# Kernel optimization log

Measured on AMD Instinct MI355X. Metric: run time of the kernel, lower is better.

The kernel has to match this reference:

```python
import jax, jax.numpy as jnp
import numpy as np

D_MODEL = 1024
NUM_HEADS = 16
D_K = D_MODEL // NUM_HEADS
THETA = 10000.0
MAX_SEQ_LEN = 2048
BATCH = 2
SEQ = 2048


def setup_inputs() -> dict:
    key = jax.random.key(0)
    ks = jax.random.split(key, 5)
    std = np.sqrt(2.0 / (D_MODEL + D_MODEL)).astype(np.float32)
    x = jax.random.normal(ks[0], (BATCH, SEQ, D_MODEL), dtype=jnp.float32)
    Wq = jax.random.normal(ks[1], (D_MODEL, D_MODEL), dtype=jnp.float32) * std
    Wk = jax.random.normal(ks[2], (D_MODEL, D_MODEL), dtype=jnp.float32) * std
    Wv = jax.random.normal(ks[3], (D_MODEL, D_MODEL), dtype=jnp.float32) * std
    Wo = jax.random.normal(ks[4], (D_MODEL, D_MODEL), dtype=jnp.float32) * std
    token_positions = jnp.arange(SEQ, dtype=jnp.int32)
    return {"x": x, "token_positions": token_positions,
            "Wq": Wq, "Wk": Wk, "Wv": Wv, "Wo": Wo}


def _rope_tables(positions):
    # freqs: [d_k/2]; angles: [seq, d_k/2]
    freqs = 1.0 / (THETA ** (jnp.arange(0, D_K, 2, dtype=jnp.float32) / D_K))
    angles = positions.astype(jnp.float32)[:, None] * freqs[None, :]
    return jnp.cos(angles), jnp.sin(angles)


def _apply_rope(t, cos, sin):
    # t: [b, h, s, d_k]; cos/sin: [s, d_k/2]; interleaved pair rotation
    x1 = t[..., 0::2]
    x2 = t[..., 1::2]
    r1 = x1 * cos - x2 * sin
    r2 = x1 * sin + x2 * cos
    return jnp.stack([r1, r2], axis=-1).reshape(t.shape)


def reference(x, token_positions, Wq, Wk, Wv, Wo):
    b, s, _ = x.shape
    # projections: y = x W^T
    q = jnp.einsum('bsi,oi->bso', x, Wq)
    k = jnp.einsum('bsi,oi->bso', x, Wk)
    v = jnp.einsum('bsi,oi->bso', x, Wv)
    # split heads: [b, h, s, d]
    q = q.reshape(b, s, NUM_HEADS, D_K).transpose(0, 2, 1, 3)
    k = k.reshape(b, s, NUM_HEADS, D_K).transpose(0, 2, 1, 3)
    v = v.reshape(b, s, NUM_HEADS, D_K).transpose(0, 2, 1, 3)
    cos, sin = _rope_tables(token_positions)
    q = _apply_rope(q, cos, sin)
    k = _apply_rope(k, cos, sin)
    scale = jnp.asarray(D_K, jnp.float32) ** 0.5
    scores = jnp.einsum('bhqd,bhkd->bhqk', q, k) / scale
    causal = jnp.tril(jnp.ones((s, s), dtype=bool))
    scores = jnp.where(causal, scores, -jnp.inf)
    attn = jax.nn.softmax(scores.astype(jnp.float32), axis=-1).astype(scores.dtype)
    out = jnp.einsum('bhqk,bhkd->bhqd', attn, v)
    out = out.transpose(0, 2, 1, 3).reshape(b, s, D_MODEL)
    return jnp.einsum('bsi,oi->bso', out, Wo)
```

## Files before the change

### kernel.cpp

```cpp
#include <hip/hip_runtime.h>
#include <stdint.h>

#define D_MODEL 1024
#define NH      16
#define DKH     64
#define SEQLEN  2048
#define BATCH   2
#define KDIM    1024

typedef __attribute__((ext_vector_type(8))) short          short8;
typedef __attribute__((ext_vector_type(4))) short          bf16x4;
typedef __attribute__((ext_vector_type(8))) unsigned short ushort8;
typedef __attribute__((ext_vector_type(4))) unsigned short usht4;
typedef __attribute__((ext_vector_type(4))) float          f32x4;

#define QSCALE 0.18033688011112042f

__device__ __forceinline__ unsigned short f2bf(float f) {
    union { float f; unsigned u; } v; v.f = f;
    unsigned u = v.u;
    unsigned r = (u + 0x7FFFu + ((u >> 16) & 1u)) >> 16;
    return (unsigned short)r;
}
__device__ __forceinline__ unsigned fbits(float f) {
    union { float f; unsigned u; } v; v.f = f; return v.u;
}

__device__ __forceinline__ void gload_lds16(const unsigned short* g, unsigned short* l) {
    __builtin_amdgcn_global_load_lds(
        (__attribute__((address_space(1))) void*)(g),
        (__attribute__((address_space(3))) void*)(l), 16, 0, 0);
}

__global__ void cvt_all(const float* __restrict__ X,  const float* __restrict__ Wq,
                        const float* __restrict__ Wk, const float* __restrict__ Wv,
                        const float* __restrict__ Wo, const int* __restrict__ pos,
                        unsigned short* __restrict__ Xb,  unsigned short* __restrict__ Wqb,
                        unsigned short* __restrict__ Wkb, unsigned short* __restrict__ Wvb,
                        unsigned short* __restrict__ Wob, float2* __restrict__ tbl) {
    const int z = blockIdx.y;
    if (z == 5) {
        int i = blockIdx.x * 256 + threadIdx.x;
        if (i < 65536) {
            int s = i >> 5, j = i & 31;
            float freq = expf(-((float)(2 * j) * (1.0f / 64.0f)) * 9.210340371976184f);
            float ang = (float)pos[s] * freq;
            float sn, cn;
            sincosf(ang, &sn, &cn);
            tbl[i] = make_float2(cn, sn);
        }
        return;
    }
    const float* src; unsigned short* dst; int n;
    if (z == 0)      { src = X;  dst = Xb;  n = 4194304; }
    else if (z == 1) { src = Wq; dst = Wqb; n = 1048576; }
    else if (z == 2) { src = Wk; dst = Wkb; n = 1048576; }
    else if (z == 3) { src = Wv; dst = Wvb; n = 1048576; }
    else             { src = Wo; dst = Wob; n = 1048576; }
    int i = (blockIdx.x * 256 + threadIdx.x) * 8;
    if (i >= n) return;
    float4 a = *(const float4*)(src + i);
    float4 b = *(const float4*)(src + i + 4);
    ushort8 o;
    o[0] = f2bf(a.x); o[1] = f2bf(a.y); o[2] = f2bf(a.z); o[3] = f2bf(a.w);
    o[4] = f2bf(b.x); o[5] = f2bf(b.y); o[6] = f2bf(b.z); o[7] = f2bf(b.w);
    *(ushort8*)(dst + i) = o;
}

__device__ __forceinline__ void gemm_core_128(
    const unsigned short* __restrict__ A, const unsigned short* __restrict__ W,
    unsigned short* a_lds, unsigned short* b_lds,
    int m0, int n0, f32x4 acc[4][4])
{
    const int tid  = threadIdx.x;
    const int lane = tid & 63;
    const int w    = tid >> 6;
    const int quad = lane >> 4;
    const int l16  = lane & 15;
    const int wm   = w & 1, wn = w >> 1;

    const int row_in = lane >> 3;
    const int cg     = ((lane & 7) ^ row_in) * 8;

    #pragma unroll
    for (int mi = 0; mi < 4; mi++)
        #pragma unroll
        for (int ni = 0; ni < 4; ni++) {
            f32x4 z = {0.f, 0.f, 0.f, 0.f};
            acc[mi][ni] = z;
        }

    const int x7 = l16 & 7;

    #pragma unroll
    for (int j = 0; j < 4; ++j) {
        int c = w * 4 + j;
        gload_lds16(A + (size_t)(m0 + c * 8 + row_in) * KDIM + cg, &a_lds[c * 512]);
        gload_lds16(W + (size_t)(n0 + c * 8 + row_in) * KDIM + cg, &b_lds[c * 512]);
    }
    __syncthreads();

    int cur = 0;
    for (int kk = 0; kk < KDIM; kk += 64) {
        if (kk + 64 < KDIM) {
            const int nxt = cur ^ 1;
            #pragma unroll
            for (int j = 0; j < 4; ++j) {
                int c = w * 4 + j;
                gload_lds16(A + (size_t)(m0 + c * 8 + row_in) * KDIM + kk + 64 + cg,
                            &a_lds[nxt * 8192 + c * 512]);
                gload_lds16(W + (size_t)(n0 + c * 8 + row_in) * KDIM + kk + 64 + cg,
                            &b_lds[nxt * 8192 + c * 512]);
            }
        }

        const unsigned short* al = &a_lds[cur * 8192];
        const unsigned short* bl = &b_lds[cur * 8192];
        short8 af[2][4], bf[2][4];
        #pragma unroll
        for (int kk2 = 0; kk2 < 2; kk2++)
            #pragma unroll
            for (int i = 0; i < 4; i++) {
                int g = (kk2 * 4 + quad) ^ x7;
                af[kk2][i] = *(const short8*)&al[(wm * 64 + i * 16 + l16) * 64 + g * 8];
                bf[kk2][i] = *(const short8*)&bl[(wn * 64 + i * 16 + l16) * 64 + g * 8];
            }
        #pragma unroll
        for (int kk2 = 0; kk2 < 2; kk2++)
            #pragma unroll
            for (int mi = 0; mi < 4; mi++)
                #pragma unroll
                for (int ni = 0; ni < 4; ni++)
                    acc[mi][ni] = __builtin_amdgcn_mfma_f32_16x16x32_bf16(af[kk2][mi], bf[kk2][ni], acc[mi][ni], 0, 0, 0);

        __syncthreads();
        cur ^= 1;
    }
}

__global__ __launch_bounds__(256, 2)
void gemm_qkv(const unsigned short* __restrict__ X,
              const unsigned short* __restrict__ Wq,
              const unsigned short* __restrict__ Wk,
              const unsigned short* __restrict__ Wv,
              const float2* __restrict__ tbl,
              unsigned short* __restrict__ q_ws,
              unsigned short* __restrict__ k_ws,
              unsigned short* __restrict__ v_ws)
{
    __shared__ __align__(16) unsigned short a_lds[2 * 128 * 64];
    __shared__ __align__(16) unsigned short b_lds[2 * 128 * 64];
    __shared__ __align__(16) unsigned short t_lds[32 * 136];

    const int z = blockIdx.z;
    const unsigned short* W = (z == 0) ? Wq : ((z == 1) ? Wk : Wv);
    const int m0 = blockIdx.x * 128, n0 = blockIdx.y * 128;

    f32x4 acc[4][4];
    gemm_core_128(X, W, a_lds, b_lds, m0, n0, acc);

    const int tid  = threadIdx.x;
    const int lane = tid & 63;
    const int w    = tid >> 6;
    const int quad = lane >> 4;
    const int l16  = lane & 15;
    const int wm   = w & 1, wn = w >> 1;

    if (z == 2) {
        const int bx = m0 >> 11;
        const int c_local_w = wn * 16 + l16;
        const int rd_c = tid >> 3;
        const int rd_s = (tid & 7) * 16;
        #pragma unroll
        for (int ni = 0; ni < 4; ni++) {
            __syncthreads();
            #pragma unroll
            for (int mi = 0; mi < 4; mi++) {
                usht4 v4;
                #pragma unroll
                for (int r = 0; r < 4; r++) v4[r] = f2bf(acc[mi][ni][r]);
                *(usht4*)&t_lds[c_local_w * 136 + wm * 64 + mi * 16 + quad * 4] = v4;
            }
            __syncthreads();
            int col = n0 + (rd_c >> 4) * 64 + ni * 16 + (rd_c & 15);
            int h = col >> 6, d = col & 63;
            size_t base = (size_t)(bx * NH + h) * DKH * SEQLEN + (size_t)d * SEQLEN
                        + (m0 & 2047) + rd_s;
            ushort8 x0 = *(ushort8*)&t_lds[rd_c * 136 + rd_s];
            ushort8 x1 = *(ushort8*)&t_lds[rd_c * 136 + rd_s + 8];
            *(ushort8*)&v_ws[base]     = x0;
            *(ushort8*)&v_ws[base + 8] = x1;
        }
    } else {
        unsigned short* dst = (z == 0) ? q_ws : k_ws;
        const float sc = (z == 0) ? QSCALE : 1.0f;
        #pragma unroll
        for (int mi = 0; mi < 4; mi++)
            #pragma unroll
            for (int ni = 0; ni < 4; ni++)
                #pragma unroll
                for (int r = 0; r < 4; r++) {
                    int row = m0 + wm * 64 + mi * 16 + quad * 4 + r;
                    int col = n0 + wn * 64 + ni * 16 + l16;
                    int b = row >> 11, s = row & 2047;
                    int h = col >> 6,  d = col & 63;
                    float val = acc[mi][ni][r];
                    float other = __shfl_xor(val, 1);
                    float2 cs = tbl[s * 32 + (d >> 1)];
                    float rv = (d & 1) ? (other * cs.y + val * cs.x)
                                       : (val * cs.x - other * cs.y);
                    dst[(size_t)(b * NH + h) * SEQLEN * DKH + (size_t)s * DKH + d] =
                        f2bf(rv * sc);
                }
    }
}

__global__ __launch_bounds__(512, 2)
void attn_kernel(const unsigned short* __restrict__ q_ws,
                 const unsigned short* __restrict__ k_ws,
                 const unsigned short* __restrict__ v_ws,
                 unsigned short* __restrict__ ao)
{
    __shared__ __align__(16) unsigned short smem[17920];
    unsigned short* k_lds = smem;
    unsigned short* v_lds = smem + 128 * 72;
    float* redO = (float*)smem;
    float* redL = redO + 8192;

    const int bh  = blockIdx.x;
    const int y   = blockIdx.y;
    const int qt2 = (y < 8) ? y : (23 - y);
    const int tid = threadIdx.x, lane = tid & 63, w = tid >> 6;
    const int quad = lane >> 4, l16 = lane & 15;
    const int g   = w >> 2;
    const int w4  = w & 3;
    const int nf0 = g * 4;

    const size_t kqbase = (size_t)bh * SEQLEN * DKH;
    const size_t vbase  = (size_t)bh * DKH * SEQLEN;
    const int b = bh >> 4, h = bh & 15;

    const int krow = tid >> 3, kcol = (tid & 7) * 8;
    const int vrow = tid >> 4, vcol = (tid & 15) * 8;

    const int q0  = qt2 * 128;
    const int nt  = qt2 + 1;
    const int qwbase = q0 + w4 * 32;

    short8 aq[2][2];
    #pragma unroll
    for (int st = 0; st < 2; st++)
        #pragma unroll
        for (int kc = 0; kc < 2; kc++)
            aq[st][kc] = *(const short8*)(q_ws + kqbase +
                (size_t)(qwbase + st * 16 + l16) * DKH + kc * 32 + quad * 8);

    f32x4 o_acc[2][4];
    #pragma unroll
    for (int st = 0; st < 2; st++)
        #pragma unroll
        for (int df = 0; df < 4; df++) { f32x4 z = {0.f,0.f,0.f,0.f}; o_acc[st][df] = z; }
    float lsum[2] = {0.f, 0.f};

    ushort8 kreg[2], vreg[2];
    #pragma unroll
    for (int rr = 0; rr < 2; ++rr) {
        kreg[rr] = *(const ushort8*)(k_ws + kqbase + (size_t)(krow + rr * 64) * DKH + kcol);
        vreg[rr] = *(const ushort8*)(v_ws + vbase + (size_t)(vrow + rr * 32) * SEQLEN + vcol);
    }

    for (int t = 0; t < nt; ++t) {
        const int s0 = t * 128;
        __syncthreads();
        #pragma unroll
        for (int rr = 0; rr < 2; ++rr) {
            *(ushort8*)&k_lds[(krow + rr * 64) * 72 + kcol]  = kreg[rr];
            *(ushort8*)&v_lds[(vrow + rr * 32) * 136 + vcol] = vreg[rr];
        }
        __syncthreads();
        if (t < nt - 1) {
            int s1 = s0 + 128;
            #pragma unroll
            for (int rr = 0; rr < 2; ++rr) {
                kreg[rr] = *(const ushort8*)(k_ws + kqbase + (size_t)(s1 + krow + rr * 64) * DKH + kcol);
                vreg[rr] = *(const ushort8*)(v_ws + vbase + (size_t)(vrow + rr * 32) * SEQLEN + s1 + vcol);
            }
        }

        const bool diag = (t == nt - 1);
        #pragma unroll
        for (int nfi = 0; nfi < 4; nfi++) {
            const int nf = nf0 + nfi;
            short8 kf0 = *(const short8*)&k_lds[(nf * 16 + l16) * 72 + 0 * 32 + quad * 8];
            short8 kf1 = *(const short8*)&k_lds[(nf * 16 + l16) * 72 + 1 * 32 + quad * 8];
            bf16x4 vf[4];
            #pragma unroll
            for (int df = 0; df < 4; df++)
                vf[df] = *(const bf16x4*)&v_lds[(df * 16 + l16) * 136 + nf * 16 + quad * 4];

            #pragma unroll
            for (int st = 0; st < 2; st++) {
                f32x4 s = {0.f,0.f,0.f,0.f};
                s = __builtin_amdgcn_mfma_f32_16x16x32_bf16(kf0, aq[st][0], s, 0, 0, 0);
                s = __builtin_amdgcn_mfma_f32_16x16x32_bf16(kf1, aq[st][1], s, 0, 0, 0);

                if (diag) {
                    int qg = qwbase + st * 16 + l16;
                    int kg = s0 + nf * 16 + quad * 4;
                    #pragma unroll
                    for (int r = 0; r < 4; r++)
                        s[r] = (kg + r <= qg) ? __builtin_amdgcn_exp2f(s[r]) : 0.f;
                } else {
                    #pragma unroll
                    for (int r = 0; r < 4; r++)
                        s[r] = __builtin_amdgcn_exp2f(s[r]);
                }
                lsum[st] += s[0] + s[1] + s[2] + s[3];

                union { unsigned u[2]; bf16x4 v; } pk;
                pk.u[0] = __builtin_amdgcn_perm(fbits(s[1]), fbits(s[0]), 0x07060302u);
                pk.u[1] = __builtin_amdgcn_perm(fbits(s[3]), fbits(s[2]), 0x07060302u);

                #pragma unroll
                for (int df = 0; df < 4; df++)
                    o_acc[st][df] = __builtin_amdgcn_mfma_f32_16x16x16bf16_1k(vf[df], pk.v, o_acc[st][df], 0, 0, 0);
            }
        }
    }

    __syncthreads();
    if (g == 1) {
        #pragma unroll
        for (int st = 0; st < 2; st++) {
            #pragma unroll
            for (int df = 0; df < 4; df++)
                *(f32x4*)&redO[(((w4 * 2 + st) * 4 + df) << 8) + lane * 4] = o_acc[st][df];
            redL[(w4 * 2 + st) * 64 + lane] = lsum[st];
        }
    }
    __syncthreads();
    if (g == 0) {
        #pragma unroll
        for (int st = 0; st < 2; st++) {
            #pragma unroll
            for (int df = 0; df < 4; df++) {
                f32x4 o1 = *(const f32x4*)&redO[(((w4 * 2 + st) * 4 + df) << 8) + lane * 4];
                o_acc[st][df] += o1;
            }
            float rs = lsum[st] + redL[(w4 * 2 + st) * 64 + lane];
            rs += __shfl_xor(rs, 16);
            rs += __shfl_xor(rs, 32);
            float inv = 1.0f / rs;
            int qg = qwbase + st * 16 + l16;
            #pragma unroll
            for (int df = 0; df < 4; df++) {
                usht4 ov;
                #pragma unroll
                for (int r = 0; r < 4; r++) ov[r] = f2bf(o_acc[st][df][r] * inv);
                *(usht4*)&ao[(size_t)(b * SEQLEN + qg) * D_MODEL + h * DKH + df * 16 + quad * 4] = ov;
            }
        }
    }
}

__global__ __launch_bounds__(256, 2)
void gemm_out(const unsigned short* __restrict__ AO,
              const unsigned short* __restrict__ Wo,
              float* __restrict__ out)
{
    __shared__ __align__(16) unsigned short a_lds[2 * 128 * 64];
    __shared__ __align__(16) unsigned short b_lds[2 * 128 * 64];

    const int m0 = blockIdx.x * 128, n0 = blockIdx.y * 128;
    f32x4 acc[4][4];
    gemm_core_128(AO, Wo, a_lds, b_lds, m0, n0, acc);

    const int lane = threadIdx.x & 63;
    const int w    = threadIdx.x >> 6;
    const int quad = lane >> 4;
    const int l16  = lane & 15;
    const int wm   = w & 1, wn = w >> 1;

    #pragma unroll
    for (int mi = 0; mi < 4; mi++)
        #pragma unroll
        for (int ni = 0; ni < 4; ni++)
            #pragma unroll
            for (int r = 0; r < 4; r++) {
                int row = m0 + wm * 64 + mi * 16 + quad * 4 + r;
                int col = n0 + wn * 64 + ni * 16 + l16;
                out[(size_t)row * D_MODEL + col] = acc[mi][ni][r];
            }
}

extern "C" void kernel_launch(void* const* d_in, const int* in_sizes, int n_in,
                              void* d_out, int out_size, void* d_ws, size_t ws_size,
                              hipStream_t stream) {
    const float* X  = (const float*)d_in[0];
    const int*   pos = (const int*)d_in[1];
    const float* Wq = (const float*)d_in[2];
    const float* Wk = (const float*)d_in[3];
    const float* Wv = (const float*)d_in[4];
    const float* Wo = (const float*)d_in[5];
    float* out = (float*)d_out;

    unsigned short* Xb  = (unsigned short*)d_ws;
    unsigned short* Wqb = Xb + 4194304;
    unsigned short* Wkb = Wqb + 1048576;
    unsigned short* Wvb = Wkb + 1048576;
    unsigned short* Wob = Wvb + 1048576;
    unsigned short* q_ws = Wob + 1048576;
    unsigned short* k_ws = q_ws + 4194304;
    unsigned short* v_ws = k_ws + 4194304;
    unsigned short* ao   = v_ws + 4194304;
    float2* tbl = (float2*)(ao + 4194304);

    cvt_all<<<dim3(2048, 6), dim3(256), 0, stream>>>(X, Wq, Wk, Wv, Wo, pos,
                                                     Xb, Wqb, Wkb, Wvb, Wob, tbl);
    gemm_qkv<<<dim3(32, 8, 3), dim3(256), 0, stream>>>(Xb, Wqb, Wkb, Wvb, tbl, q_ws, k_ws, v_ws);
    attn_kernel<<<dim3(32, 16), dim3(512), 0, stream>>>(q_ws, k_ws, v_ws, ao);
    gemm_out<<<dim3(32, 8), dim3(256), 0, stream>>>(ao, Wob, out);
}
```

Baseline: 176.2 us.

## Single-buffer QKV GEMM core and use 128x64 tiles for output projection

```diff
diff --git a/kernel.cpp b/kernel.cpp
--- a/kernel.cpp
+++ b/kernel.cpp
@@ -92,10 +92,68 @@
 
     const int x7 = l16 & 7;
 
+    for (int kk = 0; kk < KDIM; kk += 64) {
+        __syncthreads();
+        #pragma unroll
+        for (int j = 0; j < 4; ++j) {
+            int c = w * 4 + j;
+            gload_lds16(A + (size_t)(m0 + c * 8 + row_in) * KDIM + kk + cg, &a_lds[c * 512]);
+            gload_lds16(W + (size_t)(n0 + c * 8 + row_in) * KDIM + kk + cg, &b_lds[c * 512]);
+        }
+        __syncthreads();
+
+        short8 af[2][4], bf[2][4];
+        #pragma unroll
+        for (int kk2 = 0; kk2 < 2; kk2++)
+            #pragma unroll
+            for (int i = 0; i < 4; i++) {
+                int g = (kk2 * 4 + quad) ^ x7;
+                af[kk2][i] = *(const short8*)&a_lds[(wm * 64 + i * 16 + l16) * 64 + g * 8];
+                bf[kk2][i] = *(const short8*)&b_lds[(wn * 64 + i * 16 + l16) * 64 + g * 8];
+            }
+        #pragma unroll
+        for (int kk2 = 0; kk2 < 2; kk2++)
+            #pragma unroll
+            for (int mi = 0; mi < 4; mi++)
+                #pragma unroll
+                for (int ni = 0; ni < 4; ni++)
+                    acc[mi][ni] = __builtin_amdgcn_mfma_f32_16x16x32_bf16(af[kk2][mi], bf[kk2][ni], acc[mi][ni], 0, 0, 0);
+    }
+}
+
+__device__ __forceinline__ void gemm_core_128x64_db(
+    const unsigned short* __restrict__ A, const unsigned short* __restrict__ W,
+    unsigned short* a_lds, unsigned short* b_lds,
+    int m0, int n0, f32x4 acc[4][2])
+{
+    const int tid  = threadIdx.x;
+    const int lane = tid & 63;
+    const int w    = tid >> 6;
+    const int quad = lane >> 4;
+    const int l16  = lane & 15;
+    const int wm   = w & 1, wn = w >> 1;
+
+    const int row_in = lane >> 3;
+    const int cg     = ((lane & 7) ^ row_in) * 8;
+
+    #pragma unroll
+    for (int mi = 0; mi < 4; mi++)
+        #pragma unroll
+        for (int ni = 0; ni < 2; ni++) {
+            f32x4 z = {0.f, 0.f, 0.f, 0.f};
+            acc[mi][ni] = z;
+        }
+
+    const int x7 = l16 & 7;
+
     #pragma unroll
     for (int j = 0; j < 4; ++j) {
         int c = w * 4 + j;
         gload_lds16(A + (size_t)(m0 + c * 8 + row_in) * KDIM + cg, &a_lds[c * 512]);
+    }
+    #pragma unroll
+    for (int j = 0; j < 2; ++j) {
+        int c = w * 2 + j;
         gload_lds16(W + (size_t)(n0 + c * 8 + row_in) * KDIM + cg, &b_lds[c * 512]);
     }
     __syncthreads();
@@ -109,28 +167,37 @@
                 int c = w * 4 + j;
                 gload_lds16(A + (size_t)(m0 + c * 8 + row_in) * KDIM + kk + 64 + cg,
                             &a_lds[nxt * 8192 + c * 512]);
+            }
+            #pragma unroll
+            for (int j = 0; j < 2; ++j) {
+                int c = w * 2 + j;
                 gload_lds16(W + (size_t)(n0 + c * 8 + row_in) * KDIM + kk + 64 + cg,
-                            &b_lds[nxt * 8192 + c * 512]);
+                            &b_lds[nxt * 4096 + c * 512]);
             }
         }
 
         const unsigned short* al = &a_lds[cur * 8192];
-        const unsigned short* bl = &b_lds[cur * 8192];
-        short8 af[2][4], bf[2][4];
-        #pragma unroll
-        for (int kk2 = 0; kk2 < 2; kk2++)
+        const unsigned short* bl = &b_lds[cur * 4096];
+        short8 af[2][4], bf[2][2];
+        #pragma unroll
+        for (int kk2 = 0; kk2 < 2; kk2++) {
             #pragma unroll
             for (int i = 0; i < 4; i++) {
                 int g = (kk2 * 4 + quad) ^ x7;
                 af[kk2][i] = *(const short8*)&al[(wm * 64 + i * 16 + l16) * 64 + g * 8];
-                bf[kk2][i] = *(const short8*)&bl[(wn * 64 + i * 16 + l16) * 64 + g * 8];
-            }
+            }
+            #pragma unroll
+            for (int i = 0; i < 2; i++) {
+                int g = (kk2 * 4 + quad) ^ x7;
+                bf[kk2][i] = *(const short8*)&bl[(wn * 32 + i * 16 + l16) * 64 + g * 8];
+            }
+        }
         #pragma unroll
         for (int kk2 = 0; kk2 < 2; kk2++)
             #pragma unroll
             for (int mi = 0; mi < 4; mi++)
                 #pragma unroll
-                for (int ni = 0; ni < 4; ni++)
+                for (int ni = 0; ni < 2; ni++)
                     acc[mi][ni] = __builtin_amdgcn_mfma_f32_16x16x32_bf16(af[kk2][mi], bf[kk2][ni], acc[mi][ni], 0, 0, 0);
 
         __syncthreads();
@@ -148,8 +215,8 @@
               unsigned short* __restrict__ k_ws,
               unsigned short* __restrict__ v_ws)
 {
-    __shared__ __align__(16) unsigned short a_lds[2 * 128 * 64];
-    __shared__ __align__(16) unsigned short b_lds[2 * 128 * 64];
+    __shared__ __align__(16) unsigned short a_lds[128 * 64];
+    __shared__ __align__(16) unsigned short b_lds[128 * 64];
     __shared__ __align__(16) unsigned short t_lds[32 * 136];
 
     const int z = blockIdx.z;
@@ -369,11 +436,11 @@
               float* __restrict__ out)
 {
     __shared__ __align__(16) unsigned short a_lds[2 * 128 * 64];
-    __shared__ __align__(16) unsigned short b_lds[2 * 128 * 64];
-
-    const int m0 = blockIdx.x * 128, n0 = blockIdx.y * 128;
-    f32x4 acc[4][4];
-    gemm_core_128(AO, Wo, a_lds, b_lds, m0, n0, acc);
+    __shared__ __align__(16) unsigned short b_lds[2 * 64 * 64];
+
+    const int m0 = blockIdx.x * 128, n0 = blockIdx.y * 64;
+    f32x4 acc[4][2];
+    gemm_core_128x64_db(AO, Wo, a_lds, b_lds, m0, n0, acc);
 
     const int lane = threadIdx.x & 63;
     const int w    = threadIdx.x >> 6;
@@ -384,11 +451,11 @@
     #pragma unroll
     for (int mi = 0; mi < 4; mi++)
         #pragma unroll
-        for (int ni = 0; ni < 4; ni++)
+        for (int ni = 0; ni < 2; ni++)
             #pragma unroll
             for (int r = 0; r < 4; r++) {
                 int row = m0 + wm * 64 + mi * 16 + quad * 4 + r;
-                int col = n0 + wn * 64 + ni * 16 + l16;
+                int col = n0 + wn * 32 + ni * 16 + l16;
                 out[(size_t)row * D_MODEL + col] = acc[mi][ni][r];
             }
 }
@@ -419,5 +486,5 @@
                                                      Xb, Wqb, Wkb, Wvb, Wob, tbl);
     gemm_qkv<<<dim3(32, 8, 3), dim3(256), 0, stream>>>(Xb, Wqb, Wkb, Wvb, tbl, q_ws, k_ws, v_ws);
     attn_kernel<<<dim3(32, 16), dim3(512), 0, stream>>>(q_ws, k_ws, v_ws, ao);
-    gemm_out<<<dim3(32, 8), dim3(256), 0, stream>>>(ao, Wob, out);
-}
+    gemm_out<<<dim3(32, 16), dim3(256), 0, stream>>>(ao, Wob, out);
+}
```

Result: faster. 163.1 us (-7.4%).
